# Kernel tuning notes

Measured on AMD Instinct MI355X. Metric: run time of the kernel, lower is better.

## Reference

```python
import jax, jax.numpy as jnp
import numpy as np

NUM_ENT = 100000
NUM_REL = 400
D_IN = 200      # emb_dim
D_OUT = 400     # emb_dim * 2
N_EDGES = 600000  # even: first half 'in' edges, second half 'out' edges
BATCH = 1024
BN_EPS = 1e-5


def ccorr(a, b):
    # circular correlation: irfft(conj(rfft(a)) * rfft(b), n=d)
    fa = jnp.fft.rfft(a, axis=-1)
    fb = jnp.fft.rfft(b, axis=-1)
    return jnp.fft.irfft(jnp.conj(fa) * fb, n=a.shape[-1], axis=-1)


def setup_inputs() -> dict:
    key = jax.random.key(0)
    ks = jax.random.split(key, 16)
    g = lambda k, s: jax.random.normal(k, s, dtype=jnp.float32) * 0.05
    head = jax.random.randint(ks[12], (BATCH,), 0, NUM_ENT)
    rela = jax.random.randint(ks[13], (BATCH,), 0, NUM_REL)
    tail = jax.random.randint(ks[14], (BATCH,), 0, NUM_ENT)
    return {
        # learned parameters
        'ent_emb': g(ks[0], (NUM_ENT, D_IN)),
        'rel_emb': g(ks[1], (NUM_REL, D_IN)),
        'in_w': g(ks[2], (D_IN, D_OUT)),
        'out_w': g(ks[3], (D_IN, D_OUT)),
        'loop_w': g(ks[4], (D_IN, D_OUT)),
        'w_rel': g(ks[5], (D_IN, D_OUT)),
        'loop_rel': g(ks[6], (1, D_IN)),
        'bias_w': jnp.zeros((D_OUT,), jnp.float32),
        'bn_gamma': jnp.ones((D_OUT,), jnp.float32),
        'bn_beta': jnp.zeros((D_OUT,), jnp.float32),
        'emb_ent_w': g(ks[7], (NUM_ENT, D_OUT)),
        'ent_bias': jnp.zeros((NUM_ENT,), jnp.float32),
        # graph / forward args
        'src': jax.random.randint(ks[8], (N_EDGES,), 0, NUM_ENT),
        'dst': jax.random.randint(ks[9], (N_EDGES,), 0, NUM_ENT),
        'edge_type': jax.random.randint(ks[10], (N_EDGES,), 0, NUM_REL),
        'edge_norm': jax.random.uniform(ks[11], (N_EDGES,), dtype=jnp.float32),
        'triples': jnp.stack([head, rela, tail], axis=1),
    }


def reference(ent_emb, rel_emb, in_w, out_w, loop_w, w_rel, loop_rel,
              bias_w, bn_gamma, bn_beta, emb_ent_w, ent_bias,
              src, dst, edge_type, edge_norm, triples):
    E = src.shape[0]
    half = E // 2
    # --- CompGCNCov layer (eval mode: dropout = identity) ---
    # edge gather + FFT circular-correlation compose
    edge_data = ccorr(ent_emb[src], rel_emb[edge_type])          # [E, D_IN]
    # per-direction weight matmul + norm scaling
    msg = jnp.concatenate([edge_data[:half] @ in_w,
                           edge_data[half:] @ out_w], axis=0)    # [E, D_OUT]
    msg = msg * edge_norm[:, None]
    # scatter-sum aggregate, then /3 (reduce_func)
    agg = jax.ops.segment_sum(msg, dst, num_segments=NUM_ENT) / 3.0
    # self-loop term
    loop = ccorr(ent_emb, jnp.broadcast_to(loop_rel, ent_emb.shape)) @ loop_w / 3.0
    x = agg + loop + bias_w
    # BatchNorm1d (training-mode batch stats, affine)
    mean = jnp.mean(x, axis=0)
    var = jnp.var(x, axis=0)
    x = (x - mean) * jax.lax.rsqrt(var + BN_EPS) * bn_gamma + bn_beta
    x = jnp.tanh(x)                                              # act
    r = rel_emb @ w_rel                                          # [NUM_REL, D_OUT]
    # --- DistMult decoder ---
    head_emb = x[triples[:, 0]]
    rela_emb = r[triples[:, 1]]
    obj = head_emb * rela_emb                                    # [B, D_OUT]
    score = jax.nn.sigmoid(obj @ emb_ent_w.T + ent_bias)         # [B, NUM_ENT]
    return score
```

## Files before the change

### kernel.cpp

```cpp
#include <hip/hip_runtime.h>
#include <hip/hip_bf16.h>

constexpr int NUM_ENT = 100000;
constexpr int NUM_REL = 400;
constexpr int D_IN    = 200;
constexpr int D_OUT   = 400;
constexpr int N_EDGES = 600000;
constexpr int HALF_E  = N_EDGES / 2;
constexpr int BATCH   = 1024;
constexpr float BN_EPS = 1e-5f;


__global__ void build_w600(const float* __restrict__ in_w,
                           const float* __restrict__ out_w,
                           const float* __restrict__ loop_w,
                           const float* __restrict__ loop_rel,
                           float* __restrict__ W600) {
    int idx = blockIdx.x * blockDim.x + threadIdx.x;
    if (idx >= 600 * D_OUT) return;
    int k = idx / D_OUT, c = idx % D_OUT;
    float v;
    if (k < 200) {
        v = in_w[k * D_OUT + c];
    } else if (k < 400) {
        v = out_w[(k - 200) * D_OUT + c];
    } else {
        int j = k - 400;
        float acc = 0.f;
        for (int kk = 0; kk < D_IN; ++kk) {
            int idx2 = j + kk;
            if (idx2 >= D_IN) idx2 -= D_IN;
            acc += loop_rel[idx2] * loop_w[kk * D_OUT + c];
        }
        v = acc;
    }
    W600[idx] = v;
}

__global__ __launch_bounds__(64) void edge_kernel(
        const float* __restrict__ ent, const float* __restrict__ rel,
        const int* __restrict__ src, const int* __restrict__ dst,
        const int* __restrict__ etype, const float* __restrict__ norm,
        float* __restrict__ P) {
    __shared__ __align__(16) float a_s[D_IN];
    __shared__ __align__(16) float b_s[2 * D_IN];
    const int e    = blockIdx.x;
    const int lane = threadIdx.x;
    const int s  = src[e];
    const int ty = etype[e];

    if (lane < 50) {
        *reinterpret_cast<float4*>(&a_s[lane * 4]) =
            *reinterpret_cast<const float4*>(&ent[(size_t)s * D_IN + lane * 4]);
    }
    for (int t4 = lane; t4 < 100; t4 += 64) {
        int o = 4 * t4;
        if (o >= D_IN) o -= D_IN;
        *reinterpret_cast<float4*>(&b_s[4 * t4]) =
            *reinterpret_cast<const float4*>(&rel[(size_t)ty * D_IN + o]);
    }
    __syncthreads();

    if (lane < 50) {
        const int k0 = lane * 4;
        float acc0 = 0.f, acc1 = 0.f, acc2 = 0.f, acc3 = 0.f;
        for (int j = 0; j < D_IN; j += 8) {
            float4 aA = *reinterpret_cast<const float4*>(&a_s[j]);
            float4 aB = *reinterpret_cast<const float4*>(&a_s[j + 4]);
            float4 b0 = *reinterpret_cast<const float4*>(&b_s[j + k0]);
            float4 b1 = *reinterpret_cast<const float4*>(&b_s[j + k0 + 4]);
            float4 b2 = *reinterpret_cast<const float4*>(&b_s[j + k0 + 8]);
            const float aw[8]  = {aA.x, aA.y, aA.z, aA.w,
                                  aB.x, aB.y, aB.z, aB.w};
            const float bw[12] = {b0.x, b0.y, b0.z, b0.w,
                                  b1.x, b1.y, b1.z, b1.w,
                                  b2.x, b2.y, b2.z, b2.w};
            #pragma unroll
            for (int m = 0; m < 8; ++m) {
                acc0 += aw[m] * bw[m + 0];
                acc1 += aw[m] * bw[m + 1];
                acc2 += aw[m] * bw[m + 2];
                acc3 += aw[m] * bw[m + 3];
            }
        }
        const float nv = norm[e];
        float* outp = P + (size_t)dst[e] * 400 + ((e < HALF_E) ? 0 : 200) + k0;
        atomicAdd(outp + 0, nv * acc0);
        atomicAdd(outp + 1, nv * acc1);
        atomicAdd(outp + 2, nv * acc2);
        atomicAdd(outp + 3, nv * acc3);
    }
}

__global__ __launch_bounds__(256) void x_gemm_stats(
        const float* __restrict__ P, const float* __restrict__ ent,
        const float* __restrict__ W, const float* __restrict__ bias,
        float* __restrict__ sum_g, float* __restrict__ ssq_g) {
    __shared__ __align__(16) float As[40][64];
    __shared__ __align__(16) float Bs[40][64];
    __shared__ float lsum[64], lssq[64];
    int tid = threadIdx.x;
    int row0 = blockIdx.x * 64;
    int col0 = blockIdx.y * 64;
    int tx = tid & 15, ty = tid >> 4;
    float acc[4][4] = {};
    for (int kc = 0; kc < 600; kc += 40) {
        #pragma unroll
        for (int i = 0; i < 10; ++i) {
            int e = tid + 256 * i;
            int rr = e / 40, kk = e % 40;
            int row = row0 + rr, k = kc + kk;
            float v = 0.f;
            if (row < NUM_ENT)
                v = (k < 400) ? P[(size_t)row * 400 + k]
                              : ent[(size_t)row * D_IN + (k - 400)];
            As[kk][rr] = v;
        }
        #pragma unroll
        for (int i = 0; i < 10; ++i) {
            int e = tid + 256 * i;
            int kk = e / 64, cc = e % 64;
            int c = col0 + cc;
            Bs[kk][cc] = (c < D_OUT) ? W[(size_t)(kc + kk) * D_OUT + c] : 0.f;
        }
        __syncthreads();
        #pragma unroll
        for (int kk = 0; kk < 40; ++kk) {
            float4 a4 = *reinterpret_cast<const float4*>(&As[kk][tx << 2]);
            float4 b4 = *reinterpret_cast<const float4*>(&Bs[kk][ty << 2]);
            const float av[4] = {a4.x, a4.y, a4.z, a4.w};
            const float bv[4] = {b4.x, b4.y, b4.z, b4.w};
            #pragma unroll
            for (int i = 0; i < 4; ++i)
                #pragma unroll
                for (int j = 0; j < 4; ++j)
                    acc[i][j] += av[i] * bv[j];
        }
        __syncthreads();
    }
    if (tid < 64) { lsum[tid] = 0.f; lssq[tid] = 0.f; }
    __syncthreads();
    #pragma unroll
    for (int j = 0; j < 4; ++j) {
        int c = col0 + (ty << 2) + j;
        if (c < D_OUT) {
            float bv = bias[c];
            float s = 0.f, q = 0.f;
            #pragma unroll
            for (int i = 0; i < 4; ++i) {
                int row = row0 + (tx << 2) + i;
                if (row < NUM_ENT) {
                    float xv = acc[i][j] * (1.f / 3.f) + bv;
                    s += xv;
                    q += xv * xv;
                }
            }
            atomicAdd(&lsum[(ty << 2) + j], s);
            atomicAdd(&lssq[(ty << 2) + j], q);
        }
    }
    __syncthreads();
    if (tid < 64) {
        int c = col0 + tid;
        if (c < D_OUT) {
            atomicAdd(&sum_g[c], lsum[tid]);
            atomicAdd(&ssq_g[c], lssq[tid]);
        }
    }
}

__global__ void bn_finalize(const float* __restrict__ sum_g,
                            const float* __restrict__ ssq_g,
                            const float* __restrict__ gamma,
                            const float* __restrict__ beta,
                            float* __restrict__ scale,
                            float* __restrict__ shift) {
    int c = blockIdx.x * blockDim.x + threadIdx.x;
    if (c < D_OUT) {
        float m = sum_g[c] * (1.f / (float)NUM_ENT);
        float v = ssq_g[c] * (1.f / (float)NUM_ENT) - m * m;
        float rs = rsqrtf(v + BN_EPS);
        float sc = gamma[c] * rs;
        scale[c] = sc;
        shift[c] = beta[c] - m * sc;
    }
}

__global__ void rel_gemm(const float* __restrict__ rel,
                         const float* __restrict__ w_rel,
                         float* __restrict__ R) {
    int idx = blockIdx.x * blockDim.x + threadIdx.x;
    if (idx >= NUM_REL * D_OUT) return;
    int i = idx / D_OUT, c = idx % D_OUT;
    float acc = 0.f;
    for (int k = 0; k < D_IN; ++k)
        acc += rel[(size_t)i * D_IN + k] * w_rel[(size_t)k * D_OUT + c];
    R[idx] = acc;
}

__global__ __launch_bounds__(256) void obj_kernel(
        const float* __restrict__ P, const float* __restrict__ ent,
        const float* __restrict__ W, const float* __restrict__ bias,
        const float* __restrict__ scale, const float* __restrict__ shift,
        const float* __restrict__ R, const int* __restrict__ triples,
        float* __restrict__ OBJ) {
    __shared__ float As[600];
    int t = blockIdx.x;
    int h  = triples[t * 3 + 0];
    int rr = triples[t * 3 + 1];
    int tid = threadIdx.x;
    for (int k = tid; k < 600; k += 256)
        As[k] = (k < 400) ? P[(size_t)h * 400 + k]
                          : ent[(size_t)h * D_IN + (k - 400)];
    __syncthreads();
    for (int c = tid; c < D_OUT; c += 256) {
        float acc = 0.f;
        for (int k = 0; k < 600; ++k)
            acc += As[k] * W[(size_t)k * D_OUT + c];
        float xv = acc * (1.f / 3.f) + bias[c];
        float nv = tanhf(xv * scale[c] + shift[c]);
        OBJ[(size_t)t * D_OUT + c] = nv * R[(size_t)rr * D_OUT + c];
    }
}

__global__ __launch_bounds__(256) void score_gemm(
        const float* __restrict__ emb, const float* __restrict__ OBJ,
        const float* __restrict__ ent_bias, float* __restrict__ out) {
    __shared__ __align__(16) float As[40][64];
    __shared__ __align__(16) float Bs[40][64];
    int tid = threadIdx.x;
    int n0 = blockIdx.x * 64;
    int t0 = blockIdx.y * 64;
    int tx = tid & 15, ty = tid >> 4;
    float acc[4][4] = {};
    for (int kc = 0; kc < D_OUT; kc += 40) {
        #pragma unroll
        for (int i = 0; i < 10; ++i) {
            int e = tid + 256 * i;
            int rr = e / 40, kk = e % 40;
            int row = n0 + rr;
            As[kk][rr] = (row < NUM_ENT)
                       ? emb[(size_t)row * D_OUT + kc + kk] : 0.f;
        }
        #pragma unroll
        for (int i = 0; i < 10; ++i) {
            int e = tid + 256 * i;
            int tt = e / 40, kk = e % 40;
            Bs[kk][tt] = OBJ[(size_t)(t0 + tt) * D_OUT + kc + kk];
        }
        __syncthreads();
        #pragma unroll
        for (int kk = 0; kk < 40; ++kk) {
            float4 a4 = *reinterpret_cast<const float4*>(&As[kk][tx << 2]);
            float4 b4 = *reinterpret_cast<const float4*>(&Bs[kk][ty << 2]);
            const float av[4] = {a4.x, a4.y, a4.z, a4.w};
            const float bv[4] = {b4.x, b4.y, b4.z, b4.w};
            #pragma unroll
            for (int i = 0; i < 4; ++i)
                #pragma unroll
                for (int j = 0; j < 4; ++j)
                    acc[i][j] += av[i] * bv[j];
        }
        __syncthreads();
    }
    int n_base = n0 + (tx << 2);
    if (n_base < NUM_ENT) {
        #pragma unroll
        for (int j = 0; j < 4; ++j) {
            int t = t0 + (ty << 2) + j;
            float4 pk;
            float r[4];
            #pragma unroll
            for (int i = 0; i < 4; ++i) {
                float logit = acc[i][j] + ent_bias[n_base + i];
                r[i] = 1.f / (1.f + __expf(-logit));
            }
            pk.x = r[0]; pk.y = r[1]; pk.z = r[2]; pk.w = r[3];
            *reinterpret_cast<float4*>(&out[(size_t)t * NUM_ENT + n_base]) = pk;
        }
    }
}

extern "C" void kernel_launch(void* const* d_in, const int* in_sizes, int n_in,
                              void* d_out, int out_size, void* d_ws, size_t ws_size,
                              hipStream_t stream) {
    const float* ent      = (const float*)d_in[0];
    const float* rel      = (const float*)d_in[1];
    const float* in_w     = (const float*)d_in[2];
    const float* out_w    = (const float*)d_in[3];
    const float* loop_w   = (const float*)d_in[4];
    const float* w_rel    = (const float*)d_in[5];
    const float* loop_rel = (const float*)d_in[6];
    const float* bias_w   = (const float*)d_in[7];
    const float* gamma    = (const float*)d_in[8];
    const float* beta     = (const float*)d_in[9];
    const float* emb      = (const float*)d_in[10];
    const float* ent_bias = (const float*)d_in[11];
    const int*   src      = (const int*)d_in[12];
    const int*   dst      = (const int*)d_in[13];
    const int*   etype    = (const int*)d_in[14];
    const float* norm     = (const float*)d_in[15];
    const int*   triples  = (const int*)d_in[16];
    float* out            = (float*)d_out;

    float* ws_f  = (float*)d_ws;
    float* P     = ws_f;
    float* W600  = P + (size_t)NUM_ENT * 400;
    float* Rmat  = W600 + 600 * D_OUT;
    float* OBJ   = Rmat + NUM_REL * D_OUT;
    float* SUM   = OBJ + (size_t)BATCH * D_OUT;
    float* SSQ   = SUM + D_OUT;
    float* SCALE = SSQ + D_OUT;
    float* SHIFT = SCALE + D_OUT;

    hipMemsetAsync(P, 0, (size_t)NUM_ENT * 400 * sizeof(float), stream);
    hipMemsetAsync(SUM, 0, 2 * D_OUT * sizeof(float), stream);

    build_w600<<<(600 * D_OUT + 255) / 256, 256, 0, stream>>>(
        in_w, out_w, loop_w, loop_rel, W600);

    edge_kernel<<<N_EDGES, 64, 0, stream>>>(ent, rel, src, dst, etype, norm, P);

    dim3 gx((NUM_ENT + 63) / 64, (D_OUT + 63) / 64);
    x_gemm_stats<<<gx, 256, 0, stream>>>(P, ent, W600, bias_w, SUM, SSQ);

    bn_finalize<<<2, 256, 0, stream>>>(SUM, SSQ, gamma, beta, SCALE, SHIFT);

    rel_gemm<<<(NUM_REL * D_OUT + 255) / 256, 256, 0, stream>>>(rel, w_rel, Rmat);

    obj_kernel<<<BATCH, 256, 0, stream>>>(P, ent, W600, bias_w, SCALE, SHIFT,
                                          Rmat, triples, OBJ);

    dim3 gs((NUM_ENT + 63) / 64, BATCH / 64);
    score_gemm<<<gs, 256, 0, stream>>>(emb, OBJ, ent_bias, out);
}
```

Baseline: 7.306 ms.

## Use 128x128 register-blocked GEMM tiles with K-major smem and batch edges per block

Both FP32 GEMMs (x_gemm_stats and score_gemm) move from 64x64 tiles with 4x4 per-thread outputs to 128x128 tiles with 8x8 per-thread outputs. Shared memory is K-contiguous with padding and filled by float4 loads, and a transposed weight copy (WT) is built so B-tile loads are vectorised. The edge kernel packs four edges into each 256-thread block to cut launch and block-scheduling overhead. In exchange, register pressure is higher and occupancy may fall, and score_gemm's output is now written with scalar stores instead of float4 stores.

```diff
diff --git a/kernel.cpp b/kernel.cpp
--- a/kernel.cpp
+++ b/kernel.cpp
@@ -11,11 +11,14 @@
 constexpr float BN_EPS = 1e-5f;
 
 
+constexpr int TS   = 44;
+
 __global__ void build_w600(const float* __restrict__ in_w,
                            const float* __restrict__ out_w,
                            const float* __restrict__ loop_w,
                            const float* __restrict__ loop_rel,
-                           float* __restrict__ W600) {
+                           float* __restrict__ W600,
+                           float* __restrict__ WT) {
     int idx = blockIdx.x * blockDim.x + threadIdx.x;
     if (idx >= 600 * D_OUT) return;
     int k = idx / D_OUT, c = idx % D_OUT;
@@ -35,28 +38,30 @@
         v = acc;
     }
     W600[idx] = v;
-}
-
-__global__ __launch_bounds__(64) void edge_kernel(
+    WT[(size_t)c * 600 + k] = v;
+}
+
+__global__ __launch_bounds__(256) void edge_kernel(
         const float* __restrict__ ent, const float* __restrict__ rel,
         const int* __restrict__ src, const int* __restrict__ dst,
         const int* __restrict__ etype, const float* __restrict__ norm,
         float* __restrict__ P) {
-    __shared__ __align__(16) float a_s[D_IN];
-    __shared__ __align__(16) float b_s[2 * D_IN];
-    const int e    = blockIdx.x;
-    const int lane = threadIdx.x;
+    __shared__ __align__(16) float a_s[4][D_IN];
+    __shared__ __align__(16) float b_s[4][2 * D_IN];
+    const int w    = threadIdx.x >> 6;
+    const int lane = threadIdx.x & 63;
+    const int e    = blockIdx.x * 4 + w;
     const int s  = src[e];
     const int ty = etype[e];
 
     if (lane < 50) {
-        *reinterpret_cast<float4*>(&a_s[lane * 4]) =
+        *reinterpret_cast<float4*>(&a_s[w][lane * 4]) =
             *reinterpret_cast<const float4*>(&ent[(size_t)s * D_IN + lane * 4]);
     }
     for (int t4 = lane; t4 < 100; t4 += 64) {
         int o = 4 * t4;
         if (o >= D_IN) o -= D_IN;
-        *reinterpret_cast<float4*>(&b_s[4 * t4]) =
+        *reinterpret_cast<float4*>(&b_s[w][4 * t4]) =
             *reinterpret_cast<const float4*>(&rel[(size_t)ty * D_IN + o]);
     }
     __syncthreads();
@@ -65,11 +70,11 @@
         const int k0 = lane * 4;
         float acc0 = 0.f, acc1 = 0.f, acc2 = 0.f, acc3 = 0.f;
         for (int j = 0; j < D_IN; j += 8) {
-            float4 aA = *reinterpret_cast<const float4*>(&a_s[j]);
-            float4 aB = *reinterpret_cast<const float4*>(&a_s[j + 4]);
-            float4 b0 = *reinterpret_cast<const float4*>(&b_s[j + k0]);
-            float4 b1 = *reinterpret_cast<const float4*>(&b_s[j + k0 + 4]);
-            float4 b2 = *reinterpret_cast<const float4*>(&b_s[j + k0 + 8]);
+            float4 aA = *reinterpret_cast<const float4*>(&a_s[w][j]);
+            float4 aB = *reinterpret_cast<const float4*>(&a_s[w][j + 4]);
+            float4 b0 = *reinterpret_cast<const float4*>(&b_s[w][j + k0]);
+            float4 b1 = *reinterpret_cast<const float4*>(&b_s[w][j + k0 + 4]);
+            float4 b2 = *reinterpret_cast<const float4*>(&b_s[w][j + k0 + 8]);
             const float aw[8]  = {aA.x, aA.y, aA.z, aA.w,
                                   aB.x, aB.y, aB.z, aB.w};
             const float bw[12] = {b0.x, b0.y, b0.z, b0.w,
@@ -94,73 +99,85 @@
 
 __global__ __launch_bounds__(256) void x_gemm_stats(
         const float* __restrict__ P, const float* __restrict__ ent,
-        const float* __restrict__ W, const float* __restrict__ bias,
+        const float* __restrict__ WT, const float* __restrict__ bias,
         float* __restrict__ sum_g, float* __restrict__ ssq_g) {
-    __shared__ __align__(16) float As[40][64];
-    __shared__ __align__(16) float Bs[40][64];
-    __shared__ float lsum[64], lssq[64];
-    int tid = threadIdx.x;
-    int row0 = blockIdx.x * 64;
-    int col0 = blockIdx.y * 64;
-    int tx = tid & 15, ty = tid >> 4;
-    float acc[4][4] = {};
+    __shared__ __align__(16) float As[128 * TS];
+    __shared__ __align__(16) float Bs[128 * TS];
+    __shared__ float lsum[128], lssq[128];
+    const int tid = threadIdx.x;
+    const int tx  = tid & 15;
+    const int tyy = tid >> 4;
+    const int row0 = blockIdx.x * 128;
+    const int col0 = blockIdx.y * 128;
+    float acc[8][8] = {};
+
     for (int kc = 0; kc < 600; kc += 40) {
-        #pragma unroll
-        for (int i = 0; i < 10; ++i) {
-            int e = tid + 256 * i;
-            int rr = e / 40, kk = e % 40;
-            int row = row0 + rr, k = kc + kk;
-            float v = 0.f;
-            if (row < NUM_ENT)
-                v = (k < 400) ? P[(size_t)row * 400 + k]
-                              : ent[(size_t)row * D_IN + (k - 400)];
-            As[kk][rr] = v;
-        }
-        #pragma unroll
-        for (int i = 0; i < 10; ++i) {
-            int e = tid + 256 * i;
-            int kk = e / 64, cc = e % 64;
-            int c = col0 + cc;
-            Bs[kk][cc] = (c < D_OUT) ? W[(size_t)(kc + kk) * D_OUT + c] : 0.f;
+        const bool fromP = (kc < 400);
+        #pragma unroll
+        for (int i = 0; i < 5; ++i) {
+            int fi = tid + 256 * i;
+            int row = fi / 10, kb = fi % 10;
+            int r = row0 + row;
+            float4 v = make_float4(0.f, 0.f, 0.f, 0.f);
+            if (r < NUM_ENT)
+                v = fromP
+                  ? *reinterpret_cast<const float4*>(&P[(size_t)r * 400 + kc + 4 * kb])
+                  : *reinterpret_cast<const float4*>(&ent[(size_t)r * D_IN + (kc - 400) + 4 * kb]);
+            *reinterpret_cast<float4*>(&As[row * TS + 4 * kb]) = v;
+        }
+        #pragma unroll
+        for (int i = 0; i < 5; ++i) {
+            int fi = tid + 256 * i;
+            int col = fi / 10, kb = fi % 10;
+            int c = col0 + col;
+            float4 v = make_float4(0.f, 0.f, 0.f, 0.f);
+            if (c < D_OUT)
+                v = *reinterpret_cast<const float4*>(&WT[(size_t)c * 600 + kc + 4 * kb]);
+            *reinterpret_cast<float4*>(&Bs[col * TS + 4 * kb]) = v;
         }
         __syncthreads();
         #pragma unroll
-        for (int kk = 0; kk < 40; ++kk) {
-            float4 a4 = *reinterpret_cast<const float4*>(&As[kk][tx << 2]);
-            float4 b4 = *reinterpret_cast<const float4*>(&Bs[kk][ty << 2]);
-            const float av[4] = {a4.x, a4.y, a4.z, a4.w};
-            const float bv[4] = {b4.x, b4.y, b4.z, b4.w};
-            #pragma unroll
-            for (int i = 0; i < 4; ++i)
+        for (int kb = 0; kb < 10; ++kb) {
+            float4 a4[8], b4[8];
+            #pragma unroll
+            for (int i = 0; i < 8; ++i)
+                a4[i] = *reinterpret_cast<const float4*>(&As[(tx + 16 * i) * TS + 4 * kb]);
+            #pragma unroll
+            for (int j = 0; j < 8; ++j)
+                b4[j] = *reinterpret_cast<const float4*>(&Bs[(tyy + 16 * j) * TS + 4 * kb]);
+            #pragma unroll
+            for (int i = 0; i < 8; ++i)
                 #pragma unroll
-                for (int j = 0; j < 4; ++j)
-                    acc[i][j] += av[i] * bv[j];
+                for (int j = 0; j < 8; ++j)
+                    acc[i][j] += a4[i].x * b4[j].x + a4[i].y * b4[j].y
+                               + a4[i].z * b4[j].z + a4[i].w * b4[j].w;
         }
         __syncthreads();
     }
-    if (tid < 64) { lsum[tid] = 0.f; lssq[tid] = 0.f; }
+
+    if (tid < 128) { lsum[tid] = 0.f; lssq[tid] = 0.f; }
     __syncthreads();
     #pragma unroll
-    for (int j = 0; j < 4; ++j) {
-        int c = col0 + (ty << 2) + j;
+    for (int j = 0; j < 8; ++j) {
+        int c = col0 + tyy + 16 * j;
         if (c < D_OUT) {
             float bv = bias[c];
             float s = 0.f, q = 0.f;
             #pragma unroll
-            for (int i = 0; i < 4; ++i) {
-                int row = row0 + (tx << 2) + i;
+            for (int i = 0; i < 8; ++i) {
+                int row = row0 + tx + 16 * i;
                 if (row < NUM_ENT) {
                     float xv = acc[i][j] * (1.f / 3.f) + bv;
                     s += xv;
                     q += xv * xv;
                 }
             }
-            atomicAdd(&lsum[(ty << 2) + j], s);
-            atomicAdd(&lssq[(ty << 2) + j], q);
+            atomicAdd(&lsum[tyy + 16 * j], s);
+            atomicAdd(&lssq[tyy + 16 * j], q);
         }
     }
     __syncthreads();
-    if (tid < 64) {
+    if (tid < 128) {
         int c = col0 + tid;
         if (c < D_OUT) {
             atomicAdd(&sum_g[c], lsum[tid]);
@@ -226,57 +243,70 @@
 __global__ __launch_bounds__(256) void score_gemm(
         const float* __restrict__ emb, const float* __restrict__ OBJ,
         const float* __restrict__ ent_bias, float* __restrict__ out) {
-    __shared__ __align__(16) float As[40][64];
-    __shared__ __align__(16) float Bs[40][64];
-    int tid = threadIdx.x;
-    int n0 = blockIdx.x * 64;
-    int t0 = blockIdx.y * 64;
-    int tx = tid & 15, ty = tid >> 4;
-    float acc[4][4] = {};
+    __shared__ __align__(16) float As[128 * TS];
+    __shared__ __align__(16) float Bs[128 * TS];
+    const int tid = threadIdx.x;
+    const int tx  = tid & 15;
+    const int tyy = tid >> 4;
+    const int n0 = blockIdx.x * 128;
+    const int t0 = blockIdx.y * 128;
+    float acc[8][8] = {};
+
     for (int kc = 0; kc < D_OUT; kc += 40) {
         #pragma unroll
-        for (int i = 0; i < 10; ++i) {
-            int e = tid + 256 * i;
-            int rr = e / 40, kk = e % 40;
-            int row = n0 + rr;
-            As[kk][rr] = (row < NUM_ENT)
-                       ? emb[(size_t)row * D_OUT + kc + kk] : 0.f;
-        }
-        #pragma unroll
-        for (int i = 0; i < 10; ++i) {
-            int e = tid + 256 * i;
-            int tt = e / 40, kk = e % 40;
-            Bs[kk][tt] = OBJ[(size_t)(t0 + tt) * D_OUT + kc + kk];
+        for (int i = 0; i < 5; ++i) {
+            int fi = tid + 256 * i;
+            int row = fi / 10, kb = fi % 10;
+            int n = n0 + row;
+            float4 v = make_float4(0.f, 0.f, 0.f, 0.f);
+            if (n < NUM_ENT)
+                v = *reinterpret_cast<const float4*>(&emb[(size_t)n * D_OUT + kc + 4 * kb]);
+            *reinterpret_cast<float4*>(&As[row * TS + 4 * kb]) = v;
+        }
+        #pragma unroll
+        for (int i = 0; i < 5; ++i) {
+            int fi = tid + 256 * i;
+            int trow = fi / 10, kb = fi % 10;
+            float4 v = *reinterpret_cast<const float4*>(
+                &OBJ[(size_t)(t0 + trow) * D_OUT + kc + 4 * kb]);
+            *reinterpret_cast<float4*>(&Bs[trow * TS + 4 * kb]) = v;
         }
         __syncthreads();
         #pragma unroll
-        for (int kk = 0; kk < 40; ++kk) {
-            float4 a4 = *reinterpret_cast<const float4*>(&As[kk][tx << 2]);
-            float4 b4 = *reinterpret_cast<const float4*>(&Bs[kk][ty << 2]);
-            const float av[4] = {a4.x, a4.y, a4.z, a4.w};
-            const float bv[4] = {b4.x, b4.y, b4.z, b4.w};
-            #pragma unroll
-            for (int i = 0; i < 4; ++i)
+        for (int kb = 0; kb < 10; ++kb) {
+            float4 a4[8], b4[8];
+            #pragma unroll
+            for (int i = 0; i < 8; ++i)
+                a4[i] = *reinterpret_cast<const float4*>(&As[(tx + 16 * i) * TS + 4 * kb]);
+            #pragma unroll
+            for (int j = 0; j < 8; ++j)
+                b4[j] = *reinterpret_cast<const float4*>(&Bs[(tyy + 16 * j) * TS + 4 * kb]);
+            #pragma unroll
+            for (int i = 0; i < 8; ++i)
                 #pragma unroll
-                for (int j = 0; j < 4; ++j)
-                    acc[i][j] += av[i] * bv[j];
+                for (int j = 0; j < 8; ++j)
+                    acc[i][j] += a4[i].x * b4[j].x + a4[i].y * b4[j].y
+                               + a4[i].z * b4[j].z + a4[i].w * b4[j].w;
         }
         __syncthreads();
     }
-    int n_base = n0 + (tx << 2);
-    if (n_base < NUM_ENT) {
-        #pragma unroll
-        for (int j = 0; j < 4; ++j) {
-            int t = t0 + (ty << 2) + j;
-            float4 pk;
-            float r[4];
-            #pragma unroll
-            for (int i = 0; i < 4; ++i) {
-                float logit = acc[i][j] + ent_bias[n_base + i];
-                r[i] = 1.f / (1.f + __expf(-logit));
+
+    float eb[8];
+    #pragma unroll
+    for (int i = 0; i < 8; ++i) {
+        int n = n0 + tx + 16 * i;
+        eb[i] = (n < NUM_ENT) ? ent_bias[n] : 0.f;
+    }
+    #pragma unroll
+    for (int j = 0; j < 8; ++j) {
+        int t = t0 + tyy + 16 * j;
+        #pragma unroll
+        for (int i = 0; i < 8; ++i) {
+            int n = n0 + tx + 16 * i;
+            if (n < NUM_ENT) {
+                float logit = acc[i][j] + eb[i];
+                out[(size_t)t * NUM_ENT + n] = 1.f / (1.f + __expf(-logit));
             }
-            pk.x = r[0]; pk.y = r[1]; pk.z = r[2]; pk.w = r[3];
-            *reinterpret_cast<float4*>(&out[(size_t)t * NUM_ENT + n_base]) = pk;
         }
     }
 }
@@ -306,7 +336,8 @@
     float* ws_f  = (float*)d_ws;
     float* P     = ws_f;
     float* W600  = P + (size_t)NUM_ENT * 400;
-    float* Rmat  = W600 + 600 * D_OUT;
+    float* WT    = W600 + 600 * D_OUT;
+    float* Rmat  = WT + 600 * D_OUT;
     float* OBJ   = Rmat + NUM_REL * D_OUT;
     float* SUM   = OBJ + (size_t)BATCH * D_OUT;
     float* SSQ   = SUM + D_OUT;
@@ -317,12 +348,12 @@
     hipMemsetAsync(SUM, 0, 2 * D_OUT * sizeof(float), stream);
 
     build_w600<<<(600 * D_OUT + 255) / 256, 256, 0, stream>>>(
-        in_w, out_w, loop_w, loop_rel, W600);
-
-    edge_kernel<<<N_EDGES, 64, 0, stream>>>(ent, rel, src, dst, etype, norm, P);
-
-    dim3 gx((NUM_ENT + 63) / 64, (D_OUT + 63) / 64);
-    x_gemm_stats<<<gx, 256, 0, stream>>>(P, ent, W600, bias_w, SUM, SSQ);
+        in_w, out_w, loop_w, loop_rel, W600, WT);
+
+    edge_kernel<<<N_EDGES / 4, 256, 0, stream>>>(ent, rel, src, dst, etype, norm, P);
+
+    dim3 gx((NUM_ENT + 127) / 128, (D_OUT + 127) / 128);
+    x_gemm_stats<<<gx, 256, 0, stream>>>(P, ent, WT, bias_w, SUM, SSQ);
 
     bn_finalize<<<2, 256, 0, stream>>>(SUM, SSQ, gamma, beta, SCALE, SHIFT);
 
@@ -331,6 +362,6 @@
     obj_kernel<<<BATCH, 256, 0, stream>>>(P, ent, W600, bias_w, SCALE, SHIFT,
                                           Rmat, triples, OBJ);
 
-    dim3 gs((NUM_ENT + 63) / 64, BATCH / 64);
+    dim3 gs((NUM_ENT + 127) / 128, BATCH / 128);
     score_gemm<<<gs, 256, 0, stream>>>(emb, OBJ, ent_bias, out);
 }
```

Result: slower. 10.84 ms (+48.4%).
